# Performance work log

Measured on AMD Instinct MI355X. Metric: run time of the kernel, lower is better.

## Reference

```python
import jax, jax.numpy as jnp
import numpy as np

# Perfect-forest re-expression of FeatureRNN's recursive tree message passing.
K, B, D = 2048, 4, 5                       # graphs (roots), branching factor, depth
ATOM, BOND, HID, OUT = 125, 12, 125, 40    # module defaults
SIZES = [K * B**d for d in range(D)]       # nodes per level: [2048,8192,32768,131072,524288]
NOFF = [0] + list(np.cumsum(SIZES))        # node offsets per level in flat node_msg
BOFF = [0] + list(np.cumsum(SIZES[1:]))    # edge offsets: bonds stored for levels 1..D-1
N_TOTAL = int(sum(SIZES))                  # 698368
E_TOTAL = N_TOTAL - K                      # 696320


def setup_inputs() -> dict:
    key = jax.random.key(0)
    k0, k1, k2, k3 = jax.random.split(key, 4)
    return {
        "node_msg": jax.random.normal(k0, (N_TOTAL, ATOM), jnp.float32),
        "bonds": jax.random.normal(k1, (E_TOTAL, BOND), jnp.float32),
        "W1": jax.random.normal(k2, (ATOM + BOND + OUT, HID), jnp.float32) * 0.05,
        "b1": jnp.zeros((HID,), jnp.float32),
        "W2": jax.random.normal(k3, (HID, OUT), jnp.float32) * 0.05,
        "b2": jnp.zeros((OUT,), jnp.float32),
    }


def _net(x, W1, b1, W2, b2):
    # nn.Sequential(Linear, LeakyReLU(0.01), Linear, LeakyReLU(0.01))
    h = jax.nn.leaky_relu(x @ W1 + b1, 0.01)
    return jax.nn.leaky_relu(h @ W2 + b2, 0.01)


def reference(node_msg, bonds, W1, b1, W2, b2):
    # Leaves: net(cat[msg, zeros(bond+out)])
    leaf_msg = node_msg[NOFF[D - 1]:NOFF[D]]                       # [n_leaf, ATOM]
    pad = jnp.zeros((SIZES[D - 1], BOND + OUT), node_msg.dtype)
    out = _net(jnp.concatenate([leaf_msg, pad], axis=1), W1, b1, W2, b2)
    # Level-synchronous upward pass (structural loop over D-1 tree levels)
    for d in range(D - 2, -1, -1):
        n_p = SIZES[d]
        msg_p = node_msg[NOFF[d]:NOFF[d + 1]]                      # [n_p, ATOM]
        bond = bonds[BOFF[d]:BOFF[d + 1]]                          # [n_p*B, BOND]
        inp = jnp.concatenate(
            [jnp.repeat(msg_p, B, axis=0), bond, out], axis=1)     # [n_p*B, 177]
        # per-parent sum over contiguous children == cat(...).sum(dim=0)
        out = _net(inp, W1, b1, W2, b2).reshape(n_p, B, OUT).sum(axis=1)
    return out  # [K, OUT]
```

## Files before the change

### kernel.cpp

```cpp
#include <hip/hip_runtime.h>
#include <hip/hip_bf16.h>
#include <cstddef>


typedef __attribute__((ext_vector_type(8))) _Float16 h8;
typedef __attribute__((ext_vector_type(4))) float f32x4;
typedef __attribute__((ext_vector_type(4))) unsigned int v4u;

static constexpr int HID = 125, OUT = 40;

__device__ __forceinline__ unsigned short f2h(float x) {
    _Float16 h = (_Float16)x;
    return __builtin_bit_cast(unsigned short, h);
}
__device__ __forceinline__ unsigned int pkh(float a, float b) {
    return (unsigned int)f2h(a) | ((unsigned int)f2h(b) << 16);
}

__global__ void prep_w1g(const float* __restrict__ W1, unsigned short* __restrict__ w1g) {
    int idx = blockIdx.x * 256 + threadIdx.x;
    if (idx >= 6 * 8 * 64 * 8) return;
    int j = idx & 7, ln = (idx >> 3) & 63, mt = (idx >> 9) & 7, kc = idx >> 12;
    int hid = mt * 16 + (ln & 15);
    int kp = kc * 32 + ((ln >> 4) << 3) + j;
    int k = (kp < 125) ? kp
          : (kp >= 128 && kp < 140) ? kp - 3
          : (kp >= 144 && kp < 184) ? kp - 7 : -1;
    float v = (k >= 0 && hid < HID) ? W1[(size_t)k * HID + hid] : 0.f;
    w1g[idx] = f2h(v);
}

__global__ void prep_w2(const float* __restrict__ W2, unsigned int* __restrict__ w2f) {
    int t = threadIdx.x;
    for (int task = t; task < 12 * 64; task += 256) {
        int ln = task & 63, fr = task >> 6;
        int kt = fr / 3, qt = fr % 3;
        int q = qt * 16 + (ln & 15);
        unsigned int w[4];
#pragma unroll
        for (int jp = 0; jp < 4; jp++) {
            unsigned short e[2];
#pragma unroll
            for (int s = 0; s < 2; s++) {
                int j = jp * 2 + s;
                int hid = kt * 32 + ((j >> 2) << 4) + ((ln >> 4) << 2) + (j & 3);
                float v = (hid < HID && q < OUT) ? W2[(size_t)hid * OUT + q] : 0.f;
                e[s] = f2h(v);
            }
            w[jp] = (unsigned int)e[0] | ((unsigned int)e[1] << 16);
        }
        v4u val = {w[0], w[1], w[2], w[3]};
        ((v4u*)w2f)[fr * 64 + ln] = val;
    }
}

__global__ void __launch_bounds__(256, 2)
leaf_k(const float* __restrict__ msg, const unsigned short* __restrict__ w1g,
       const unsigned int* __restrict__ w2f,
       const float* __restrict__ b1, const float* __restrict__ b2,
       unsigned short* __restrict__ outp) {
    __shared__ float Xs[4][4000];

    const int tid = threadIdx.x;
    const int lane = tid & 63;
    const int wv = tid >> 6;
    const int l15 = tid & 15;
    const int l16 = (tid >> 4) & 3;
    const int row0 = blockIdx.x * 128 + wv * 32;

    {
        const f32x4* src = (const f32x4*)(msg + (size_t)row0 * 125);
        f32x4* dst = (f32x4*)&Xs[wv][0];
#pragma unroll
        for (int i = 0; i < 16; i++) {
            int u = lane + i * 64;
            if (i < 15 || u < 1000) dst[u] = src[u];
        }
    }

    f32x4 acc[8][2];
#pragma unroll
    for (int mt = 0; mt < 8; mt++) {
        f32x4 bi;
#pragma unroll
        for (int r = 0; r < 4; r++) {
            int h_ = mt * 16 + l16 * 4 + r;
            bi[r] = (h_ < HID) ? b1[h_] : 0.f;
        }
        acc[mt][0] = bi;
        acc[mt][1] = bi;
    }

#pragma unroll
    for (int j = 0; j < 4; ++j) {
        h8 xf[2];
#pragma unroll
        for (int nt = 0; nt < 2; ++nt) {
            const float* rp = &Xs[wv][(nt * 16 + l15) * 125];
            const int k0 = j * 32 + l16 * 8;
            float t[8];
#pragma unroll
            for (int i = 0; i < 8; i++) {
                int col = k0 + i;
                int cs = (col < 125) ? col : 0;
                float v = rp[cs];
                t[i] = (col < 125) ? v : 0.f;
            }
            v4u xv = {pkh(t[0], t[1]), pkh(t[2], t[3]), pkh(t[4], t[5]), pkh(t[6], t[7])};
            xf[nt] = __builtin_bit_cast(h8, xv);
        }
#pragma unroll
        for (int mt = 0; mt < 8; ++mt) {
            h8 wf = *(const h8*)&w1g[(size_t)((j * 8 + mt) * 64 + lane) * 8];
            acc[mt][0] = __builtin_amdgcn_mfma_f32_16x16x32_f16(wf, xf[0], acc[mt][0], 0, 0, 0);
            acc[mt][1] = __builtin_amdgcn_mfma_f32_16x16x32_f16(wf, xf[1], acc[mt][1], 0, 0, 0);
        }
    }

#pragma unroll
    for (int mt = 0; mt < 8; mt++)
#pragma unroll
        for (int nt = 0; nt < 2; nt++)
#pragma unroll
            for (int r = 0; r < 4; r++)
                acc[mt][nt][r] = fmaxf(acc[mt][nt][r], 0.01f * acc[mt][nt][r]);

    float b2v[3];
#pragma unroll
    for (int qt = 0; qt < 3; qt++) {
        int q = qt * 16 + l15;
        b2v[qt] = (q < OUT) ? b2[q] : 0.f;
    }

    unsigned short* s16 = (unsigned short*)&Xs[wv][0];
#pragma unroll
    for (int nt = 0; nt < 2; ++nt) {
        h8 A[4];
#pragma unroll
        for (int kt = 0; kt < 4; kt++) {
            v4u av = {pkh(acc[2 * kt][nt][0], acc[2 * kt][nt][1]),
                      pkh(acc[2 * kt][nt][2], acc[2 * kt][nt][3]),
                      pkh(acc[2 * kt + 1][nt][0], acc[2 * kt + 1][nt][1]),
                      pkh(acc[2 * kt + 1][nt][2], acc[2 * kt + 1][nt][3])};
            A[kt] = __builtin_bit_cast(h8, av);
        }
#pragma unroll
        for (int qt = 0; qt < 3; ++qt) {
            f32x4 o = {0.f, 0.f, 0.f, 0.f};
#pragma unroll
            for (int kt = 0; kt < 4; kt++) {
                v4u wvv = ((const v4u*)w2f)[(kt * 3 + qt) * 64 + lane];
                o = __builtin_amdgcn_mfma_f32_16x16x32_f16(
                    A[kt], __builtin_bit_cast(h8, wvv), o, 0, 0, 0);
            }
            int q = qt * 16 + l15;
            if (q < OUT) {
#pragma unroll
                for (int r = 0; r < 4; r++) {
                    int rl = nt * 16 + l16 * 4 + r;
                    float v = o[r] + b2v[qt];
                    v = fmaxf(v, 0.01f * v);
                    s16[rl * 40 + q] = f2h(v);
                }
            }
        }
    }
    {
        v4u* gdst = (v4u*)(outp + (size_t)row0 * 40);
        const v4u* s4 = (const v4u*)s16;
#pragma unroll
        for (int i = 0; i < 3; i++) {
            int u = lane + i * 64;
            if (i < 2 || u < 160) gdst[u] = s4[u];
        }
    }
}

template <int MODE>
__global__ void __launch_bounds__(256, 4)
mid_k(const float* __restrict__ msg, const float* __restrict__ bonds,
      const unsigned short* __restrict__ child,
      const unsigned short* __restrict__ w1g, const unsigned int* __restrict__ w2f,
      const float* __restrict__ b1, const float* __restrict__ b2,
      void* __restrict__ outp) {
    __shared__ float MS[4][1000];
    __shared__ float BS[4][384];
    __shared__ unsigned short CS[4][1280];

    const int tid = threadIdx.x;
    const int lane = tid & 63;
    const int wv = tid >> 6;
    const int l15 = tid & 15;
    const int l16 = (tid >> 4) & 3;
    const int row0 = blockIdx.x * 128 + wv * 32;
    const int par0 = row0 >> 2;

    {
        const f32x4* sm = (const f32x4*)(msg + (size_t)par0 * 125);
        f32x4* dm = (f32x4*)&MS[wv][0];
#pragma unroll
        for (int i = 0; i < 4; i++) {
            int u = lane + i * 64;
            if (i < 3 || u < 250) dm[u] = sm[u];
        }
        const f32x4* sb = (const f32x4*)(bonds + (size_t)row0 * 12);
        f32x4* db = (f32x4*)&BS[wv][0];
#pragma unroll
        for (int i = 0; i < 2; i++) {
            int u = lane + i * 64;
            if (i < 1 || u < 96) db[u] = sb[u];
        }
        const v4u* sc = (const v4u*)(child + (size_t)row0 * 40);
        v4u* dc = (v4u*)&CS[wv][0];
#pragma unroll
        for (int i = 0; i < 3; i++) {
            int u = lane + i * 64;
            if (i < 2 || u < 160) dc[u] = sc[u];
        }
    }

    f32x4 acc[8][2];
#pragma unroll
    for (int mt = 0; mt < 8; mt++) {
        f32x4 bi;
#pragma unroll
        for (int r = 0; r < 4; r++) {
            int h_ = mt * 16 + l16 * 4 + r;
            bi[r] = (h_ < HID) ? b1[h_] : 0.f;
        }
        acc[mt][0] = bi;
        acc[mt][1] = bi;
    }

#pragma unroll
    for (int j = 0; j < 6; ++j) {
        h8 xf[2];
#pragma unroll
        for (int nt = 0; nt < 2; ++nt) {
            const int rl = nt * 16 + l15;
            if (j < 4) {
                const float* pp = &MS[wv][(rl >> 2) * 125];
                const int k0 = j * 32 + l16 * 8;
                float t[8];
#pragma unroll
                for (int i = 0; i < 8; i++) {
                    int col = k0 + i;
                    int cs = (col < 125) ? col : 0;
                    float v = pp[cs];
                    t[i] = (col < 125) ? v : 0.f;
                }
                v4u xv = {pkh(t[0], t[1]), pkh(t[2], t[3]), pkh(t[4], t[5]), pkh(t[6], t[7])};
                xf[nt] = __builtin_bit_cast(h8, xv);
            } else if (j == 4) {
                if (l16 < 2) {
                    const float* bp = &BS[wv][rl * 12];
                    float t[8];
#pragma unroll
                    for (int i = 0; i < 8; i++) {
                        int c = l16 * 8 + i;
                        int cs = (c < 12) ? c : 0;
                        float v = bp[cs];
                        t[i] = (c < 12) ? v : 0.f;
                    }
                    v4u xv = {pkh(t[0], t[1]), pkh(t[2], t[3]), pkh(t[4], t[5]), pkh(t[6], t[7])};
                    xf[nt] = __builtin_bit_cast(h8, xv);
                } else {
                    xf[nt] = *(const h8*)&CS[wv][rl * 40 + (l16 - 2) * 8];
                }
            } else {
                if (l16 < 3) {
                    xf[nt] = *(const h8*)&CS[wv][rl * 40 + 16 + l16 * 8];
                } else {
                    h8 z = {};
                    xf[nt] = z;
                }
            }
        }
#pragma unroll
        for (int mt = 0; mt < 8; ++mt) {
            h8 wf = *(const h8*)&w1g[(size_t)((j * 8 + mt) * 64 + lane) * 8];
            acc[mt][0] = __builtin_amdgcn_mfma_f32_16x16x32_f16(wf, xf[0], acc[mt][0], 0, 0, 0);
            acc[mt][1] = __builtin_amdgcn_mfma_f32_16x16x32_f16(wf, xf[1], acc[mt][1], 0, 0, 0);
        }
    }

#pragma unroll
    for (int mt = 0; mt < 8; mt++)
#pragma unroll
        for (int nt = 0; nt < 2; nt++)
#pragma unroll
            for (int r = 0; r < 4; r++)
                acc[mt][nt][r] = fmaxf(acc[mt][nt][r], 0.01f * acc[mt][nt][r]);

    float b2v[3];
#pragma unroll
    for (int qt = 0; qt < 3; qt++) {
        int q = qt * 16 + l15;
        b2v[qt] = (q < OUT) ? b2[q] : 0.f;
    }
#pragma unroll
    for (int nt = 0; nt < 2; ++nt) {
        h8 A[4];
#pragma unroll
        for (int kt = 0; kt < 4; kt++) {
            v4u av = {pkh(acc[2 * kt][nt][0], acc[2 * kt][nt][1]),
                      pkh(acc[2 * kt][nt][2], acc[2 * kt][nt][3]),
                      pkh(acc[2 * kt + 1][nt][0], acc[2 * kt + 1][nt][1]),
                      pkh(acc[2 * kt + 1][nt][2], acc[2 * kt + 1][nt][3])};
            A[kt] = __builtin_bit_cast(h8, av);
        }
#pragma unroll
        for (int qt = 0; qt < 3; ++qt) {
            f32x4 o = {0.f, 0.f, 0.f, 0.f};
#pragma unroll
            for (int kt = 0; kt < 4; kt++) {
                v4u wvv = ((const v4u*)w2f)[(kt * 3 + qt) * 64 + lane];
                o = __builtin_amdgcn_mfma_f32_16x16x32_f16(
                    A[kt], __builtin_bit_cast(h8, wvv), o, 0, 0, 0);
            }
            int q = qt * 16 + l15;
            float s = 0.f;
#pragma unroll
            for (int r = 0; r < 4; r++) {
                float v = o[r] + b2v[qt];
                s += fmaxf(v, 0.01f * v);
            }
            if (q < OUT) {
                int p = par0 + nt * 4 + l16;
                if (MODE == 1)
                    ((unsigned short*)outp)[(size_t)p * 40 + q] = f2h(s);
                else
                    ((float*)outp)[(size_t)p * 40 + q] = s;
            }
        }
    }
}

extern "C" void kernel_launch(void* const* d_in, const int* in_sizes, int n_in,
                              void* d_out, int out_size, void* d_ws, size_t ws_size,
                              hipStream_t stream) {
    const float* node_msg = (const float*)d_in[0];
    const float* bonds = (const float*)d_in[1];
    const float* W1 = (const float*)d_in[2];
    const float* b1 = (const float*)d_in[3];
    const float* W2 = (const float*)d_in[4];
    const float* b2 = (const float*)d_in[5];
    float* out = (float*)d_out;

    char* ws = (char*)d_ws;
    unsigned short* bufA = (unsigned short*)ws;
    unsigned short* bufB = (unsigned short*)(ws + 41943040);
    unsigned short* w1g = (unsigned short*)(ws + 52428800);
    unsigned int* w2f = (unsigned int*)(ws + 52428800 + 49152);

    prep_w1g<<<96, 256, 0, stream>>>(W1, w1g);
    prep_w2<<<1, 256, 0, stream>>>(W2, w2f);

    leaf_k<<<4096, 256, 0, stream>>>(
        node_msg + (size_t)175104 * 125, w1g, w2f, b1, b2, bufA);
    mid_k<1><<<4096, 256, 0, stream>>>(
        node_msg + (size_t)43008 * 125, bonds + (size_t)172032 * 12, bufA,
        w1g, w2f, b1, b2, bufB);
    mid_k<1><<<1024, 256, 0, stream>>>(
        node_msg + (size_t)10240 * 125, bonds + (size_t)40960 * 12, bufB,
        w1g, w2f, b1, b2, bufA);
    mid_k<1><<<256, 256, 0, stream>>>(
        node_msg + (size_t)2048 * 125, bonds + (size_t)8192 * 12, bufA,
        w1g, w2f, b1, b2, bufB);
    mid_k<2><<<64, 256, 0, stream>>>(
        node_msg, bonds, bufB, w1g, w2f, b1, b2, out);
}
```

Measured before the change: 201.9 us.

## Stream leaf input through double-buffered LDS chunks overlapped with MFMA

The leaf kernel no longer stages each wave's full 32x125 fp32 tile into shared memory before computing. Each 32-column chunk is now loaded into registers, written into one of two small padded LDS buffers, and the next chunk's global loads are issued while the MFMAs for the current chunk run. This cuts LDS use per block, which lets launch bounds ask for 3 blocks per SM instead of 2, and is meant to hide global load latency. The cost is scalar per-lane loads in place of 16-byte vector loads, and the later s16 reuse of the now smaller shared buffer has to fit. An output index expression is rewritten to an equivalent form.

```diff
diff --git a/kernel.cpp b/kernel.cpp
--- a/kernel.cpp
+++ b/kernel.cpp
@@ -54,29 +54,40 @@
     }
 }
 
-__global__ void __launch_bounds__(256, 2)
+__global__ void __launch_bounds__(256, 3)
 leaf_k(const float* __restrict__ msg, const unsigned short* __restrict__ w1g,
        const unsigned int* __restrict__ w2f,
        const float* __restrict__ b1, const float* __restrict__ b2,
        unsigned short* __restrict__ outp) {
-    __shared__ float Xs[4][4000];
+    __shared__ float Xs[4][2][32 * 36];
 
     const int tid = threadIdx.x;
     const int lane = tid & 63;
     const int wv = tid >> 6;
     const int l15 = tid & 15;
     const int l16 = (tid >> 4) & 3;
+    const int sr = lane >> 5;
+    const int sc = lane & 31;
     const int row0 = blockIdx.x * 128 + wv * 32;
 
-    {
-        const f32x4* src = (const f32x4*)(msg + (size_t)row0 * 125);
-        f32x4* dst = (f32x4*)&Xs[wv][0];
-#pragma unroll
-        for (int i = 0; i < 16; i++) {
-            int u = lane + i * 64;
-            if (i < 15 || u < 1000) dst[u] = src[u];
-        }
-    }
+    float xr[16];
+
+    auto issue = [&](int j) {
+        const int col = j * 32 + sc;
+        const bool ok = col < 125;
+#pragma unroll
+        for (int q = 0; q < 16; q++) {
+            int r = 2 * q + sr;
+            xr[q] = ok ? msg[(size_t)(row0 + r) * 125 + col] : 0.f;
+        }
+    };
+    auto writes = [&](int j, int b) {
+#pragma unroll
+        for (int q = 0; q < 16; q++) {
+            int r = 2 * q + sr;
+            Xs[wv][b][r * 36 + sc] = xr[q];
+        }
+    };
 
     f32x4 acc[8][2];
 #pragma unroll
@@ -91,30 +102,31 @@
         acc[mt][1] = bi;
     }
 
+    issue(0);
+    writes(0, 0);
 #pragma unroll
     for (int j = 0; j < 4; ++j) {
-        h8 xf[2];
-#pragma unroll
-        for (int nt = 0; nt < 2; ++nt) {
-            const float* rp = &Xs[wv][(nt * 16 + l15) * 125];
-            const int k0 = j * 32 + l16 * 8;
-            float t[8];
-#pragma unroll
-            for (int i = 0; i < 8; i++) {
-                int col = k0 + i;
-                int cs = (col < 125) ? col : 0;
-                float v = rp[cs];
-                t[i] = (col < 125) ? v : 0.f;
-            }
-            v4u xv = {pkh(t[0], t[1]), pkh(t[2], t[3]), pkh(t[4], t[5]), pkh(t[6], t[7])};
-            xf[nt] = __builtin_bit_cast(h8, xv);
-        }
-#pragma unroll
-        for (int mt = 0; mt < 8; ++mt) {
-            h8 wf = *(const h8*)&w1g[(size_t)((j * 8 + mt) * 64 + lane) * 8];
-            acc[mt][0] = __builtin_amdgcn_mfma_f32_16x16x32_f16(wf, xf[0], acc[mt][0], 0, 0, 0);
-            acc[mt][1] = __builtin_amdgcn_mfma_f32_16x16x32_f16(wf, xf[1], acc[mt][1], 0, 0, 0);
-        }
+        if (j + 1 < 4) issue(j + 1);
+        {
+            h8 xf[2];
+#pragma unroll
+            for (int nt = 0; nt < 2; ++nt) {
+                const float* rp = &Xs[wv][j & 1][(nt * 16 + l15) * 36 + l16 * 8];
+                float t[8];
+#pragma unroll
+                for (int i = 0; i < 8; i++) t[i] = rp[i];
+                v4u xv = {pkh(t[0], t[1]), pkh(t[2], t[3]),
+                          pkh(t[4], t[5]), pkh(t[6], t[7])};
+                xf[nt] = __builtin_bit_cast(h8, xv);
+            }
+#pragma unroll
+            for (int mt = 0; mt < 8; ++mt) {
+                h8 wf = *(const h8*)&w1g[(size_t)((j * 8 + mt) * 64 + lane) * 8];
+                acc[mt][0] = __builtin_amdgcn_mfma_f32_16x16x32_f16(wf, xf[0], acc[mt][0], 0, 0, 0);
+                acc[mt][1] = __builtin_amdgcn_mfma_f32_16x16x32_f16(wf, xf[1], acc[mt][1], 0, 0, 0);
+            }
+        }
+        if (j + 1 < 4) writes(j + 1, (j + 1) & 1);
     }
 
 #pragma unroll
@@ -132,7 +144,7 @@
         b2v[qt] = (q < OUT) ? b2[q] : 0.f;
     }
 
-    unsigned short* s16 = (unsigned short*)&Xs[wv][0];
+    unsigned short* s16 = (unsigned short*)&Xs[wv][0][0];
 #pragma unroll
     for (int nt = 0; nt < 2; ++nt) {
         h8 A[4];
@@ -326,7 +338,7 @@
                 s += fmaxf(v, 0.01f * v);
             }
             if (q < OUT) {
-                int p = par0 + nt * 4 + l16;
+                int p = par0 + (nt * 16 + l16 * 4) / 4;
                 if (MODE == 1)
                     ((unsigned short*)outp)[(size_t)p * 40 + q] = f2h(s);
                 else
```

Result: no change. 202.6 us (+0.4%).
